# Kernel optimization log

Hardware: AMD Instinct MI355X
Metric: run time of the kernel (lower is better)

Reference implementation:

```python
import jax, jax.numpy as jnp
import numpy as np

EMB = 64  # emb_dim
T = 4     # message-passing steps


def setup_inputs() -> dict:
    key = jax.random.key(0)
    ks = jax.random.split(key, 9)
    B, N = 32, 1024
    graph = jax.random.uniform(ks[0], (B, N, N), jnp.float32)   # dense adjacency/weights
    Xv = jax.random.normal(ks[1], (B, N, 1), jnp.float32)       # per-vertex scalar feature
    s = lambda k, shp: (jax.random.normal(k, shp, jnp.float32) * 0.05)
    return {
        "graph": graph,
        "Xv": Xv,
        "W1": s(ks[2], (EMB, 1)),        # Linear(1, emb) no bias, torch layout [out, in]
        "W2": s(ks[3], (EMB, EMB)),
        "W3": s(ks[4], (EMB, EMB)),
        "W4": s(ks[5], (EMB, 1)),
        "W5": s(ks[6], (1, 2 * EMB)),
        "W6": s(ks[7], (EMB, EMB)),
        "W7": s(ks[8], (EMB, EMB)),
    }


def reference(graph, Xv, W1, W2, W3, W4, W5, W6, W7):
    B, N = Xv.shape[0], Xv.shape[1]
    # v1 = W1(Xv): [B,N,1] @ [1,EMB] -> [B,N,EMB]
    v1 = Xv @ W1.T
    # Original: v3 = W3(sum_j W4(graph[...,None])). W4 is linear (no bias), so
    # sum_j W4(g_ij) == W4(sum_j g_ij) -- exact by linearity, avoids [B,N,N,EMB] temp.
    deg = jnp.sum(graph, axis=2, keepdims=True)        # [B,N,1]
    v3 = (deg @ W4.T) @ W3.T                           # [B,N,EMB]
    base = v1 + v3                                     # loop-invariant part
    emb = jnp.zeros((B, N, EMB), dtype=Xv.dtype)
    for _ in range(T):
        neighbor_sum = jnp.einsum('bij,bjd->bid', graph, emb)  # bmm aggregation
        emb = jax.nn.relu(base + neighbor_sum @ W2.T)
    emb_sum = jnp.sum(emb, axis=1)                     # [B,EMB]
    # v6.repeat(1,N).view(B,N,EMB) == broadcast the per-graph vector to every vertex
    v6 = jnp.broadcast_to((emb_sum @ W6.T)[:, None, :], (B, N, EMB))
    v7 = emb @ W7.T
    ct = jax.nn.relu(jnp.concatenate([v6, v7], axis=2))  # [B,N,2*EMB]
    return (ct @ W5.T)[..., 0]                            # [B,N]
```

## Files before the change

kernel.cpp:

```cpp
#include <hip/hip_runtime.h>
#include <stdint.h>

#define BATCH 32
#define NV 1024
#define EMB 64

typedef __attribute__((ext_vector_type(8))) short bf16x8;
typedef __attribute__((ext_vector_type(4))) float f32x4;

__device__ __forceinline__ unsigned short f2b(float f) {
  unsigned int u = __builtin_bit_cast(unsigned int, f);
  u += 0x7fffu + ((u >> 16) & 1u);
  return (unsigned short)(u >> 16);
}
__device__ __forceinline__ float b2f(unsigned short s) {
  unsigned int u = ((unsigned int)s) << 16;
  return __builtin_bit_cast(float, u);
}

__device__ __forceinline__ void gll16(void* lds, const void* gsrc) {
  __builtin_amdgcn_global_load_lds(
      (const __attribute__((address_space(1))) unsigned int*)gsrc,
      (__attribute__((address_space(3))) unsigned int*)lds, 16, 0, 0);
}

__global__ __launch_bounds__(256) void k_prep(
    const float* __restrict__ graph, const float* __restrict__ Xv,
    const float* __restrict__ W1, const float* __restrict__ W3,
    const float* __restrict__ W4,
    unsigned short* __restrict__ G16, float* __restrict__ degp,
    float* __restrict__ w34g, unsigned short* __restrict__ embT)
{
  __shared__ float w34s[EMB];
  __shared__ __align__(16) unsigned short ebT[EMB][68];
  const int tid = threadIdx.x;
  const int b = blockIdx.x >> 4;
  const int rb = blockIdx.x & 15;
  if (tid < EMB) {
    float s = 0.f;
    const float* w3r = W3 + tid * EMB;
#pragma unroll
    for (int k = 0; k < EMB; ++k) s += w3r[k] * W4[k];
    w34s[tid] = s;
    if (blockIdx.x == 0) w34g[tid] = s;
  }
  __syncthreads();
  const int wv = tid >> 6, lane = tid & 63;
  const float w1v = W1[lane];
  const float w34v = w34s[lane];
  for (int i = 0; i < 16; ++i) {
    const int row = rb * 64 + wv * 16 + i;
    const float4* gr = (const float4*)(graph + ((size_t)b * NV + row) * NV);
    float part = 0.f;
    ushort4 outp[4];
#pragma unroll
    for (int c = 0; c < 4; ++c) {
      float4 v = gr[c * 64 + lane];
      part += (v.x + v.y) + (v.z + v.w);
      outp[c].x = f2b(v.x); outp[c].y = f2b(v.y);
      outp[c].z = f2b(v.z); outp[c].w = f2b(v.w);
    }
    ushort4* g16r = (ushort4*)(G16 + ((size_t)b * NV + row) * NV);
#pragma unroll
    for (int c = 0; c < 4; ++c) g16r[c * 64 + lane] = outp[c];
#pragma unroll
    for (int d = 1; d < 64; d <<= 1) part += __shfl_xor(part, d);
    const float deg = part;
    if (lane == 0) degp[b * NV + row] = deg;
    const float xv = Xv[b * NV + row];
    const float bs = xv * w1v + deg * w34v;
    ebT[lane][wv * 16 + i] = f2b(fmaxf(bs, 0.f));
  }
  __syncthreads();
  const int e = tid >> 2, q = tid & 3;
  ushort4* dst = (ushort4*)(embT + ((size_t)(b * EMB + e)) * NV + rb * 64 + q * 16);
  const ushort4* srcr = (const ushort4*)(&ebT[e][q * 16]);
#pragma unroll
  for (int c = 0; c < 4; ++c) dst[c] = srcr[c];
}

__global__ __launch_bounds__(256) void k_step(
    const unsigned short* __restrict__ G16,
    const unsigned short* __restrict__ embin,
    unsigned short* __restrict__ embout,
    const float* __restrict__ W2, const float* __restrict__ W1,
    const float* __restrict__ w34g, const float* __restrict__ Xv,
    const float* __restrict__ degp)
{
  __shared__ __align__(16) char lds[16384];
  char* At = lds;
  char* Bt = lds + 8192;
  const int tid = threadIdx.x;
  const int lane = tid & 63;
  const int wv = tid >> 6;
  const int wm = wv >> 1;
  const int wn = wv & 1;
  const int b = blockIdx.x >> 4;
  const int mblk = blockIdx.x & 15;
  const int l15 = lane & 15, l4 = lane >> 4;

  bf16x8 w2f[2][2];
  float w1e[2], w34e[2];
#pragma unroll
  for (int e16 = 0; e16 < 2; ++e16) {
    const int eg = wn * 32 + e16 * 16 + l15;
    w1e[e16] = W1[eg];
    w34e[e16] = w34g[eg];
#pragma unroll
    for (int kk = 0; kk < 2; ++kk) {
      const float* src = W2 + eg * 64 + kk * 32 + l4 * 8;
      bf16x8 f;
#pragma unroll
      for (int j = 0; j < 8; ++j) f[j] = (short)f2b(src[j]);
      w2f[e16][kk] = f;
    }
  }

  f32x4 acc[2][2] = {};
  const size_t gbase = ((size_t)b * NV + mblk * 64) * NV;
  const size_t ebase = (size_t)b * EMB * NV;

  for (int kt = 0; kt < 16; ++kt) {
#pragma unroll
    for (int i = 0; i < 2; ++i) {
      const int cc = i * 256 + tid;
      const int lrow = cc >> 3, lcg = cc & 7;
      const int gcg = lcg ^ (lrow & 7);
      gll16(At + (i * 256 + wv * 64) * 16,
            G16 + gbase + (size_t)lrow * NV + kt * 64 + gcg * 8);
    }
#pragma unroll
    for (int i = 0; i < 2; ++i) {
      const int cc = i * 256 + tid;
      const int er = cc >> 3, lcg = cc & 7;
      const int gcg = lcg ^ (er & 7);
      gll16(Bt + (i * 256 + wv * 64) * 16,
            embin + ebase + (size_t)er * NV + kt * 64 + gcg * 8);
    }
    __syncthreads();
#pragma unroll
    for (int kk = 0; kk < 2; ++kk) {
      bf16x8 af[2], bf[2];
      const int gq = kk * 4 + l4;
#pragma unroll
      for (int m16 = 0; m16 < 2; ++m16) {
        const int row = wm * 32 + m16 * 16 + l15;
        af[m16] = *(const bf16x8*)(At + row * 128 + ((gq ^ (row & 7)) << 4));
      }
#pragma unroll
      for (int n16 = 0; n16 < 2; ++n16) {
        const int er = wn * 32 + n16 * 16 + l15;
        bf[n16] = *(const bf16x8*)(Bt + er * 128 + ((gq ^ (er & 7)) << 4));
      }
#pragma unroll
      for (int m16 = 0; m16 < 2; ++m16)
#pragma unroll
        for (int n16 = 0; n16 < 2; ++n16)
          acc[m16][n16] = __builtin_amdgcn_mfma_f32_16x16x32_bf16(
              af[m16], bf[n16], acc[m16][n16], 0, 0, 0);
    }
    __syncthreads();
  }

#pragma unroll
  for (int m16 = 0; m16 < 2; ++m16)
#pragma unroll
    for (int n16 = 0; n16 < 2; ++n16)
#pragma unroll
      for (int r = 0; r < 4; ++r) {
        const int m = wm * 32 + m16 * 16 + l4 * 4 + r;
        const int n = wn * 32 + n16 * 16 + l15;
        const int addr = m * 128 + (((n >> 3) ^ (m & 7)) << 4) + (n & 7) * 2;
        *(unsigned short*)(At + addr) = f2b(acc[m16][n16][r]);
      }
  __syncthreads();

  f32x4 acc2[2][2] = {};
#pragma unroll
  for (int kk = 0; kk < 2; ++kk) {
    bf16x8 sa[2];
    const int gq = kk * 4 + l4;
#pragma unroll
    for (int m16 = 0; m16 < 2; ++m16) {
      const int row = wm * 32 + m16 * 16 + l15;
      sa[m16] = *(const bf16x8*)(At + row * 128 + ((gq ^ (row & 7)) << 4));
    }
#pragma unroll
    for (int m16 = 0; m16 < 2; ++m16)
#pragma unroll
      for (int e16 = 0; e16 < 2; ++e16)
        acc2[m16][e16] = __builtin_amdgcn_mfma_f32_16x16x32_bf16(
            sa[m16], w2f[e16][kk], acc2[m16][e16], 0, 0, 0);
  }

#pragma unroll
  for (int m16 = 0; m16 < 2; ++m16) {
    const int m0 = mblk * 64 + wm * 32 + m16 * 16 + l4 * 4;
    float xv[4], dg[4];
#pragma unroll
    for (int r = 0; r < 4; ++r) {
      xv[r] = Xv[b * NV + m0 + r];
      dg[r] = degp[b * NV + m0 + r];
    }
#pragma unroll
    for (int e16 = 0; e16 < 2; ++e16) {
      const int eg = wn * 32 + e16 * 16 + l15;
      ushort4 pk;
      unsigned short* pks = (unsigned short*)&pk;
#pragma unroll
      for (int r = 0; r < 4; ++r) {
        const float bs = xv[r] * w1e[e16] + dg[r] * w34e[e16];
        pks[r] = f2b(fmaxf(acc2[m16][e16][r] + bs, 0.f));
      }
      *(ushort4*)(embout + ((size_t)(b * EMB + eg)) * NV + m0) = pk;
    }
  }
}

__global__ __launch_bounds__(256) void k_red(
    const unsigned short* __restrict__ embT, const float* __restrict__ W6,
    const float* __restrict__ W5, float* __restrict__ s6)
{
  __shared__ float part[256];
  __shared__ float esum[EMB];
  const int b = blockIdx.x, tid = threadIdx.x;
  const int e = tid >> 2, q = tid & 3;
  const unsigned short* rowp = embT + ((size_t)(b * EMB + e)) * NV;
  float s = 0.f;
  for (int j = 0; j < 32; ++j) {
    const ushort4* p = (const ushort4*)(rowp + q * 8 + j * 32);
    ushort4 a = p[0], c = p[1];
    s += (b2f(a.x) + b2f(a.y)) + (b2f(a.z) + b2f(a.w)) +
         (b2f(c.x) + b2f(c.y)) + (b2f(c.z) + b2f(c.w));
  }
  part[tid] = s;
  __syncthreads();
  if (tid < EMB)
    esum[tid] = part[tid * 4] + part[tid * 4 + 1] + part[tid * 4 + 2] + part[tid * 4 + 3];
  __syncthreads();
  if (tid < EMB) {
    float v6 = 0.f;
    const float* w6r = W6 + tid * EMB;
#pragma unroll
    for (int k = 0; k < EMB; ++k) v6 += w6r[k] * esum[k];
    float contrib = W5[tid] * fmaxf(v6, 0.f);
#pragma unroll
    for (int d = 1; d < 64; d <<= 1) contrib += __shfl_xor(contrib, d);
    if (tid == 0) s6[b] = contrib;
  }
}

__global__ __launch_bounds__(256) void k_out(
    const unsigned short* __restrict__ embT, const float* __restrict__ W7,
    const float* __restrict__ W5, const float* __restrict__ s6,
    float* __restrict__ out)
{
  __shared__ __align__(16) unsigned short et[EMB][256];
  const int tid = threadIdx.x;
  const int b = blockIdx.x >> 2;
  const int n0 = (blockIdx.x & 3) * 256;
#pragma unroll
  for (int i = 0; i < 8; ++i) {
    const int c = i * 256 + tid;
    const int k = c >> 5, off = (c & 31) * 8;
    *(uint4*)&et[k][off] =
        *(const uint4*)(embT + ((size_t)(b * EMB + k)) * NV + n0 + off);
  }
  __syncthreads();
  float ev[64];
#pragma unroll
  for (int k = 0; k < 64; ++k) ev[k] = b2f(et[k][tid]);
  float s7 = 0.f;
  for (int e = 0; e < 64; ++e) {
    const float* w7r = W7 + e * 64;
    float a = 0.f;
#pragma unroll
    for (int k = 0; k < 64; ++k) a += ev[k] * w7r[k];
    s7 += W5[64 + e] * fmaxf(a, 0.f);
  }
  out[b * NV + n0 + tid] = s6[b] + s7;
}

extern "C" void kernel_launch(void* const* d_in, const int* in_sizes, int n_in,
                              void* d_out, int out_size, void* d_ws, size_t ws_size,
                              hipStream_t stream) {
  const float* graph = (const float*)d_in[0];
  const float* Xv = (const float*)d_in[1];
  const float* W1 = (const float*)d_in[2];
  const float* W2 = (const float*)d_in[3];
  const float* W3 = (const float*)d_in[4];
  const float* W4 = (const float*)d_in[5];
  const float* W5 = (const float*)d_in[6];
  const float* W6 = (const float*)d_in[7];
  const float* W7 = (const float*)d_in[8];
  float* out = (float*)d_out;
  char* ws = (char*)d_ws;

  unsigned short* G16 = (unsigned short*)ws;
  unsigned short* embA = (unsigned short*)(ws + 67108864);
  unsigned short* embB = (unsigned short*)(ws + 71303168);
  float* degp = (float*)(ws + 75497472);
  float* w34g = (float*)(ws + 75628544);
  float* s6 = (float*)(ws + 75628800);

  k_prep<<<512, 256, 0, stream>>>(graph, Xv, W1, W3, W4, G16, degp, w34g, embA);
  k_step<<<512, 256, 0, stream>>>(G16, embA, embB, W2, W1, w34g, Xv, degp);
  k_step<<<512, 256, 0, stream>>>(G16, embB, embA, W2, W1, w34g, Xv, degp);
  k_step<<<512, 256, 0, stream>>>(G16, embA, embB, W2, W1, w34g, Xv, degp);
  k_red<<<32, 256, 0, stream>>>(embB, W6, W5, s6);
  k_out<<<128, 256, 0, stream>>>(embB, W7, W5, s6, out);
}
```

Measured before the change: 309.8 us.

## Fuse all stages into one persistent kernel with grid barriers and double buffering

Replaces the six launches (prep, three steps, reduce, output) with one persistent kernel of 512 blocks that synchronises between message-passing steps using an atomic-counter grid barrier. The step GEMM's LDS staging is double-buffered so the next tile's loads overlap the current MFMA work. Degree, Xv and W3·W4 are kept in LDS, and the final step keeps its embeddings in LDS to compute the readout directly. The graph-sum reduction uses atomics into a zeroed workspace. This removes launch gaps and intermediate global traffic, but relies on all 512 blocks being co-resident (launch bounds of 2 blocks per SM) and adds a memset plus spin-wait barrier costs.

New measurement: 483.5 us. +56.1%, slower.

```diff
diff --git a/kernel.cpp b/kernel.cpp
--- a/kernel.cpp
+++ b/kernel.cpp
@@ -1,9 +1,9 @@
 #include <hip/hip_runtime.h>
 #include <stdint.h>
 
-#define BATCH 32
 #define NV 1024
 #define EMB 64
+#define NBLK 512
 
 typedef __attribute__((ext_vector_type(8))) short bf16x8;
 typedef __attribute__((ext_vector_type(4))) float f32x4;
@@ -24,80 +24,93 @@
       (__attribute__((address_space(3))) unsigned int*)lds, 16, 0, 0);
 }
 
-__global__ __launch_bounds__(256) void k_prep(
+__global__ __launch_bounds__(256, 2) void k_fused(
     const float* __restrict__ graph, const float* __restrict__ Xv,
-    const float* __restrict__ W1, const float* __restrict__ W3,
-    const float* __restrict__ W4,
-    unsigned short* __restrict__ G16, float* __restrict__ degp,
-    float* __restrict__ w34g, unsigned short* __restrict__ embT)
+    const float* __restrict__ W1, const float* __restrict__ W2,
+    const float* __restrict__ W3, const float* __restrict__ W4,
+    const float* __restrict__ W5, const float* __restrict__ W6,
+    const float* __restrict__ W7,
+    unsigned short* __restrict__ G16,
+    unsigned short* __restrict__ embA,
+    unsigned short* __restrict__ embB,
+    float* __restrict__ esum_ws, unsigned int* __restrict__ bar,
+    float* __restrict__ out)
 {
+  __shared__ __align__(16) char ldsbuf[32768];
   __shared__ float w34s[EMB];
-  __shared__ __align__(16) unsigned short ebT[EMB][68];
+  __shared__ float degs[EMB];
+  __shared__ float xvs[EMB];
+  __shared__ float esl[EMB];
+  __shared__ float redl[256];
+  __shared__ float s6l;
+
   const int tid = threadIdx.x;
+  const int lane = tid & 63;
+  const int wv = tid >> 6;
   const int b = blockIdx.x >> 4;
-  const int rb = blockIdx.x & 15;
+  const int mb = blockIdx.x & 15;
+  const int wm = wv >> 1, wn = wv & 1;
+  const int l15 = lane & 15, l4 = lane >> 4;
+
+  auto gbar = [&](unsigned int target) {
+    __syncthreads();
+    if (tid == 0) {
+      __threadfence();
+      __hip_atomic_fetch_add(bar, 1u, __ATOMIC_RELAXED, __HIP_MEMORY_SCOPE_AGENT);
+      while (__hip_atomic_load(bar, __ATOMIC_RELAXED, __HIP_MEMORY_SCOPE_AGENT) < target)
+        __builtin_amdgcn_s_sleep(2);
+      __threadfence();
+    }
+    __syncthreads();
+  };
+
   if (tid < EMB) {
     float s = 0.f;
     const float* w3r = W3 + tid * EMB;
 #pragma unroll
     for (int k = 0; k < EMB; ++k) s += w3r[k] * W4[k];
     w34s[tid] = s;
-    if (blockIdx.x == 0) w34g[tid] = s;
   }
   __syncthreads();
-  const int wv = tid >> 6, lane = tid & 63;
-  const float w1v = W1[lane];
-  const float w34v = w34s[lane];
-  for (int i = 0; i < 16; ++i) {
-    const int row = rb * 64 + wv * 16 + i;
-    const float4* gr = (const float4*)(graph + ((size_t)b * NV + row) * NV);
-    float part = 0.f;
-    ushort4 outp[4];
-#pragma unroll
-    for (int c = 0; c < 4; ++c) {
-      float4 v = gr[c * 64 + lane];
-      part += (v.x + v.y) + (v.z + v.w);
-      outp[c].x = f2b(v.x); outp[c].y = f2b(v.y);
-      outp[c].z = f2b(v.z); outp[c].w = f2b(v.w);
-    }
-    ushort4* g16r = (ushort4*)(G16 + ((size_t)b * NV + row) * NV);
-#pragma unroll
-    for (int c = 0; c < 4; ++c) g16r[c * 64 + lane] = outp[c];
-#pragma unroll
-    for (int d = 1; d < 64; d <<= 1) part += __shfl_xor(part, d);
-    const float deg = part;
-    if (lane == 0) degp[b * NV + row] = deg;
-    const float xv = Xv[b * NV + row];
-    const float bs = xv * w1v + deg * w34v;
-    ebT[lane][wv * 16 + i] = f2b(fmaxf(bs, 0.f));
-  }
-  __syncthreads();
-  const int e = tid >> 2, q = tid & 3;
-  ushort4* dst = (ushort4*)(embT + ((size_t)(b * EMB + e)) * NV + rb * 64 + q * 16);
-  const ushort4* srcr = (const ushort4*)(&ebT[e][q * 16]);
-#pragma unroll
-  for (int c = 0; c < 4; ++c) dst[c] = srcr[c];
-}
-
-__global__ __launch_bounds__(256) void k_step(
-    const unsigned short* __restrict__ G16,
-    const unsigned short* __restrict__ embin,
-    unsigned short* __restrict__ embout,
-    const float* __restrict__ W2, const float* __restrict__ W1,
-    const float* __restrict__ w34g, const float* __restrict__ Xv,
-    const float* __restrict__ degp)
-{
-  __shared__ __align__(16) char lds[16384];
-  char* At = lds;
-  char* Bt = lds + 8192;
-  const int tid = threadIdx.x;
-  const int lane = tid & 63;
-  const int wv = tid >> 6;
-  const int wm = wv >> 1;
-  const int wn = wv & 1;
-  const int b = blockIdx.x >> 4;
-  const int mblk = blockIdx.x & 15;
-  const int l15 = lane & 15, l4 = lane >> 4;
+  {
+    unsigned short* ebT = (unsigned short*)ldsbuf;
+    const float w1v = W1[lane];
+    const float w34v = w34s[lane];
+    for (int i = 0; i < 16; ++i) {
+      const int rloc = wv * 16 + i;
+      const int row = mb * 64 + rloc;
+      const float4* gr = (const float4*)(graph + ((size_t)b * NV + row) * NV);
+      float part = 0.f;
+      ushort4 outp[4];
+#pragma unroll
+      for (int c = 0; c < 4; ++c) {
+        float4 v = gr[c * 64 + lane];
+        part += (v.x + v.y) + (v.z + v.w);
+        outp[c].x = f2b(v.x); outp[c].y = f2b(v.y);
+        outp[c].z = f2b(v.z); outp[c].w = f2b(v.w);
+      }
+      ushort4* g16r = (ushort4*)(G16 + ((size_t)b * NV + row) * NV);
+#pragma unroll
+      for (int c = 0; c < 4; ++c) g16r[c * 64 + lane] = outp[c];
+#pragma unroll
+      for (int d = 1; d < 64; d <<= 1) part += __shfl_xor(part, d);
+      const float deg = part;
+      const float xv = Xv[b * NV + row];
+      if (lane == 0) { degs[rloc] = deg; xvs[rloc] = xv; }
+      const float bs = xv * w1v + deg * w34v;
+      ebT[lane * 68 + rloc] = f2b(fmaxf(bs, 0.f));
+    }
+    __syncthreads();
+    const int e = tid >> 2, q = tid & 3;
+    ushort4* dst = (ushort4*)(embA + ((size_t)(b * EMB + e)) * NV + mb * 64 + q * 16);
+    const ushort4* srcr = (const ushort4*)(ebT + e * 68 + q * 16);
+#pragma unroll
+    for (int c = 0; c < 4; ++c) dst[c] = srcr[c];
+  }
+  gbar(NBLK);
+
+  const size_t gbase = ((size_t)b * NV + mb * 64) * NV;
+  const size_t ebase = (size_t)b * EMB * NV;
 
   bf16x8 w2f[2][2];
   float w1e[2], w34e[2];
@@ -105,7 +118,7 @@
   for (int e16 = 0; e16 < 2; ++e16) {
     const int eg = wn * 32 + e16 * 16 + l15;
     w1e[e16] = W1[eg];
-    w34e[e16] = w34g[eg];
+    w34e[e16] = w34s[eg];
 #pragma unroll
     for (int kk = 0; kk < 2; ++kk) {
       const float* src = W2 + eg * 64 + kk * 32 + l4 * 8;
@@ -116,169 +129,174 @@
     }
   }
 
-  f32x4 acc[2][2] = {};
-  const size_t gbase = ((size_t)b * NV + mblk * 64) * NV;
-  const size_t ebase = (size_t)b * EMB * NV;
-
-  for (int kt = 0; kt < 16; ++kt) {
-#pragma unroll
-    for (int i = 0; i < 2; ++i) {
-      const int cc = i * 256 + tid;
-      const int lrow = cc >> 3, lcg = cc & 7;
-      const int gcg = lcg ^ (lrow & 7);
-      gll16(At + (i * 256 + wv * 64) * 16,
-            G16 + gbase + (size_t)lrow * NV + kt * 64 + gcg * 8);
-    }
-#pragma unroll
-    for (int i = 0; i < 2; ++i) {
-      const int cc = i * 256 + tid;
-      const int er = cc >> 3, lcg = cc & 7;
-      const int gcg = lcg ^ (er & 7);
-      gll16(Bt + (i * 256 + wv * 64) * 16,
-            embin + ebase + (size_t)er * NV + kt * 64 + gcg * 8);
-    }
-    __syncthreads();
+  auto do_step = [&](const unsigned short* embin, unsigned short* embout, int s) {
+    f32x4 acc[2][2] = {};
+    auto STAGE = [&](int bufi, int kt) {
+      char* Ad = ldsbuf + bufi * 16384;
+      char* Bd = Ad + 8192;
+#pragma unroll
+      for (int i = 0; i < 2; ++i) {
+        const int cc = i * 256 + tid;
+        const int lrow = cc >> 3, lcg = cc & 7;
+        const int gcg = lcg ^ (lrow & 7);
+        gll16(Ad + (i * 256 + wv * 64) * 16,
+              G16 + gbase + (size_t)lrow * NV + kt * 64 + gcg * 8);
+      }
+#pragma unroll
+      for (int i = 0; i < 2; ++i) {
+        const int cc = i * 256 + tid;
+        const int er = cc >> 3, lcg = cc & 7;
+        const int gcg = lcg ^ (er & 7);
+        gll16(Bd + (i * 256 + wv * 64) * 16,
+              embin + ebase + (size_t)er * NV + kt * 64 + gcg * 8);
+      }
+    };
+    STAGE(0, 0);
+    int cur = 0;
+    for (int kt = 0; kt < 16; ++kt) {
+      if (kt < 15) {
+        STAGE(cur ^ 1, kt + 1);
+        asm volatile("s_waitcnt vmcnt(4)" ::: "memory");
+      } else {
+        asm volatile("s_waitcnt vmcnt(0)" ::: "memory");
+      }
+      __builtin_amdgcn_s_barrier();
+      asm volatile("" ::: "memory");
+      const char* At = ldsbuf + cur * 16384;
+      const char* Bt = At + 8192;
+#pragma unroll
+      for (int kk = 0; kk < 2; ++kk) {
+        bf16x8 af[2], bf[2];
+        const int gq = kk * 4 + l4;
+#pragma unroll
+        for (int m16 = 0; m16 < 2; ++m16) {
+          const int row = wm * 32 + m16 * 16 + l15;
+          af[m16] = *(const bf16x8*)(At + row * 128 + ((gq ^ (row & 7)) << 4));
+        }
+#pragma unroll
+        for (int n16 = 0; n16 < 2; ++n16) {
+          const int er = wn * 32 + n16 * 16 + l15;
+          bf[n16] = *(const bf16x8*)(Bt + er * 128 + ((gq ^ (er & 7)) << 4));
+        }
+#pragma unroll
+        for (int m16 = 0; m16 < 2; ++m16)
+#pragma unroll
+          for (int n16 = 0; n16 < 2; ++n16)
+            acc[m16][n16] = __builtin_amdgcn_mfma_f32_16x16x32_bf16(
+                af[m16], bf[n16], acc[m16][n16], 0, 0, 0);
+      }
+      asm volatile("" ::: "memory");
+      __builtin_amdgcn_s_barrier();
+      cur ^= 1;
+    }
+
+    char* St = ldsbuf;
+    if (s == 3 && tid < 64) esl[tid] = 0.f;
+#pragma unroll
+    for (int m16 = 0; m16 < 2; ++m16)
+#pragma unroll
+      for (int n16 = 0; n16 < 2; ++n16)
+#pragma unroll
+        for (int r = 0; r < 4; ++r) {
+          const int m = wm * 32 + m16 * 16 + l4 * 4 + r;
+          const int n = wn * 32 + n16 * 16 + l15;
+          const int addr = m * 128 + (((n >> 3) ^ (m & 7)) << 4) + (n & 7) * 2;
+          *(unsigned short*)(St + addr) = f2b(acc[m16][n16][r]);
+        }
+    __syncthreads();
+
+    f32x4 acc2[2][2] = {};
 #pragma unroll
     for (int kk = 0; kk < 2; ++kk) {
-      bf16x8 af[2], bf[2];
+      bf16x8 sa[2];
       const int gq = kk * 4 + l4;
 #pragma unroll
       for (int m16 = 0; m16 < 2; ++m16) {
         const int row = wm * 32 + m16 * 16 + l15;
-        af[m16] = *(const bf16x8*)(At + row * 128 + ((gq ^ (row & 7)) << 4));
-      }
-#pragma unroll
-      for (int n16 = 0; n16 < 2; ++n16) {
-        const int er = wn * 32 + n16 * 16 + l15;
-        bf[n16] = *(const bf16x8*)(Bt + er * 128 + ((gq ^ (er & 7)) << 4));
+        sa[m16] = *(const bf16x8*)(St + row * 128 + ((gq ^ (row & 7)) << 4));
       }
 #pragma unroll
       for (int m16 = 0; m16 < 2; ++m16)
 #pragma unroll
-        for (int n16 = 0; n16 < 2; ++n16)
-          acc[m16][n16] = __builtin_amdgcn_mfma_f32_16x16x32_bf16(
-              af[m16], bf[n16], acc[m16][n16], 0, 0, 0);
-    }
-    __syncthreads();
-  }
-
-#pragma unroll
-  for (int m16 = 0; m16 < 2; ++m16)
-#pragma unroll
-    for (int n16 = 0; n16 < 2; ++n16)
-#pragma unroll
-      for (int r = 0; r < 4; ++r) {
-        const int m = wm * 32 + m16 * 16 + l4 * 4 + r;
-        const int n = wn * 32 + n16 * 16 + l15;
-        const int addr = m * 128 + (((n >> 3) ^ (m & 7)) << 4) + (n & 7) * 2;
-        *(unsigned short*)(At + addr) = f2b(acc[m16][n16][r]);
-      }
-  __syncthreads();
-
-  f32x4 acc2[2][2] = {};
-#pragma unroll
-  for (int kk = 0; kk < 2; ++kk) {
-    bf16x8 sa[2];
-    const int gq = kk * 4 + l4;
+        for (int e16 = 0; e16 < 2; ++e16)
+          acc2[m16][e16] = __builtin_amdgcn_mfma_f32_16x16x32_bf16(
+              sa[m16], w2f[e16][kk], acc2[m16][e16], 0, 0, 0);
+    }
+
+    float* et = (float*)(ldsbuf + 8192);
 #pragma unroll
     for (int m16 = 0; m16 < 2; ++m16) {
-      const int row = wm * 32 + m16 * 16 + l15;
-      sa[m16] = *(const bf16x8*)(At + row * 128 + ((gq ^ (row & 7)) << 4));
-    }
-#pragma unroll
-    for (int m16 = 0; m16 < 2; ++m16)
-#pragma unroll
-      for (int e16 = 0; e16 < 2; ++e16)
-        acc2[m16][e16] = __builtin_amdgcn_mfma_f32_16x16x32_bf16(
-            sa[m16], w2f[e16][kk], acc2[m16][e16], 0, 0, 0);
-  }
-
-#pragma unroll
-  for (int m16 = 0; m16 < 2; ++m16) {
-    const int m0 = mblk * 64 + wm * 32 + m16 * 16 + l4 * 4;
-    float xv[4], dg[4];
-#pragma unroll
-    for (int r = 0; r < 4; ++r) {
-      xv[r] = Xv[b * NV + m0 + r];
-      dg[r] = degp[b * NV + m0 + r];
-    }
-#pragma unroll
-    for (int e16 = 0; e16 < 2; ++e16) {
-      const int eg = wn * 32 + e16 * 16 + l15;
-      ushort4 pk;
-      unsigned short* pks = (unsigned short*)&pk;
-#pragma unroll
-      for (int r = 0; r < 4; ++r) {
-        const float bs = xv[r] * w1e[e16] + dg[r] * w34e[e16];
-        pks[r] = f2b(fmaxf(acc2[m16][e16][r] + bs, 0.f));
-      }
-      *(ushort4*)(embout + ((size_t)(b * EMB + eg)) * NV + m0) = pk;
-    }
-  }
-}
-
-__global__ __launch_bounds__(256) void k_red(
-    const unsigned short* __restrict__ embT, const float* __restrict__ W6,
-    const float* __restrict__ W5, float* __restrict__ s6)
-{
-  __shared__ float part[256];
-  __shared__ float esum[EMB];
-  const int b = blockIdx.x, tid = threadIdx.x;
-  const int e = tid >> 2, q = tid & 3;
-  const unsigned short* rowp = embT + ((size_t)(b * EMB + e)) * NV;
-  float s = 0.f;
-  for (int j = 0; j < 32; ++j) {
-    const ushort4* p = (const ushort4*)(rowp + q * 8 + j * 32);
-    ushort4 a = p[0], c = p[1];
-    s += (b2f(a.x) + b2f(a.y)) + (b2f(a.z) + b2f(a.w)) +
-         (b2f(c.x) + b2f(c.y)) + (b2f(c.z) + b2f(c.w));
-  }
-  part[tid] = s;
-  __syncthreads();
-  if (tid < EMB)
-    esum[tid] = part[tid * 4] + part[tid * 4 + 1] + part[tid * 4 + 2] + part[tid * 4 + 3];
-  __syncthreads();
-  if (tid < EMB) {
+      const int ml0 = wm * 32 + m16 * 16 + l4 * 4;
+      float xv4[4], dg4[4];
+#pragma unroll
+      for (int r = 0; r < 4; ++r) { xv4[r] = xvs[ml0 + r]; dg4[r] = degs[ml0 + r]; }
+#pragma unroll
+      for (int e16 = 0; e16 < 2; ++e16) {
+        const int eg = wn * 32 + e16 * 16 + l15;
+        if (s < 3) {
+          ushort4 pk;
+          unsigned short* pks = (unsigned short*)&pk;
+#pragma unroll
+          for (int r = 0; r < 4; ++r) {
+            const float bs = xv4[r] * w1e[e16] + dg4[r] * w34e[e16];
+            pks[r] = f2b(fmaxf(acc2[m16][e16][r] + bs, 0.f));
+          }
+          *(ushort4*)(embout + ((size_t)(b * EMB + eg)) * NV + mb * 64 + ml0) = pk;
+        } else {
+          float evs = 0.f;
+#pragma unroll
+          for (int r = 0; r < 4; ++r) {
+            const float bs = xv4[r] * w1e[e16] + dg4[r] * w34e[e16];
+            const float val = fmaxf(acc2[m16][e16][r] + bs, 0.f);
+            et[(ml0 + r) * 65 + eg] = val;
+            evs += val;
+          }
+          atomicAdd(&esl[eg], evs);
+        }
+      }
+    }
+    if (s == 3) {
+      __syncthreads();
+      if (tid < 64) atomicAdd(&esum_ws[b * EMB + tid], esl[tid]);
+    }
+  };
+
+  do_step(embA, embB, 1);  gbar(2 * NBLK);
+  do_step(embB, embA, 2);  gbar(3 * NBLK);
+  do_step(embA, embB, 3);  gbar(4 * NBLK);
+
+  if (tid < 64) {
+    const float* es = esum_ws + b * EMB;
     float v6 = 0.f;
     const float* w6r = W6 + tid * EMB;
 #pragma unroll
-    for (int k = 0; k < EMB; ++k) v6 += w6r[k] * esum[k];
-    float contrib = W5[tid] * fmaxf(v6, 0.f);
-#pragma unroll
-    for (int d = 1; d < 64; d <<= 1) contrib += __shfl_xor(contrib, d);
-    if (tid == 0) s6[b] = contrib;
-  }
-}
-
-__global__ __launch_bounds__(256) void k_out(
-    const unsigned short* __restrict__ embT, const float* __restrict__ W7,
-    const float* __restrict__ W5, const float* __restrict__ s6,
-    float* __restrict__ out)
-{
-  __shared__ __align__(16) unsigned short et[EMB][256];
-  const int tid = threadIdx.x;
-  const int b = blockIdx.x >> 2;
-  const int n0 = (blockIdx.x & 3) * 256;
-#pragma unroll
-  for (int i = 0; i < 8; ++i) {
-    const int c = i * 256 + tid;
-    const int k = c >> 5, off = (c & 31) * 8;
-    *(uint4*)&et[k][off] =
-        *(const uint4*)(embT + ((size_t)(b * EMB + k)) * NV + n0 + off);
+    for (int k = 0; k < EMB; ++k) v6 += w6r[k] * es[k];
+    float c = W5[tid] * fmaxf(v6, 0.f);
+#pragma unroll
+    for (int d = 1; d < 64; d <<= 1) c += __shfl_xor(c, d);
+    if (tid == 0) s6l = c;
   }
   __syncthreads();
-  float ev[64];
-#pragma unroll
-  for (int k = 0; k < 64; ++k) ev[k] = b2f(et[k][tid]);
-  float s7 = 0.f;
-  for (int e = 0; e < 64; ++e) {
-    const float* w7r = W7 + e * 64;
-    float a = 0.f;
-#pragma unroll
-    for (int k = 0; k < 64; ++k) a += ev[k] * w7r[k];
-    s7 += W5[64 + e] * fmaxf(a, 0.f);
-  }
-  out[b * NV + n0 + tid] = s6[b] + s7;
+  {
+    const float* et = (const float*)(ldsbuf + 8192);
+    const int v = tid & 63, eq = tid >> 6;
+    float ev[64];
+#pragma unroll
+    for (int k = 0; k < EMB; ++k) ev[k] = et[v * 65 + k];
+    float sp = 0.f;
+    for (int e = eq * 16; e < eq * 16 + 16; ++e) {
+      const float* w7r = W7 + e * 64;
+      float a = 0.f;
+#pragma unroll
+      for (int k = 0; k < 64; ++k) a += ev[k] * w7r[k];
+      sp += W5[64 + e] * fmaxf(a, 0.f);
+    }
+    redl[tid] = sp;
+    __syncthreads();
+    if (tid < 64)
+      out[b * NV + mb * 64 + tid] =
+          s6l + redl[tid] + redl[tid + 64] + redl[tid + 128] + redl[tid + 192];
+  }
 }
 
 extern "C" void kernel_launch(void* const* d_in, const int* in_sizes, int n_in,
@@ -297,16 +315,13 @@
   char* ws = (char*)d_ws;
 
   unsigned short* G16 = (unsigned short*)ws;
-  unsigned short* embA = (unsigned short*)(ws + 67108864);
-  unsigned short* embB = (unsigned short*)(ws + 71303168);
-  float* degp = (float*)(ws + 75497472);
-  float* w34g = (float*)(ws + 75628544);
-  float* s6 = (float*)(ws + 75628800);
-
-  k_prep<<<512, 256, 0, stream>>>(graph, Xv, W1, W3, W4, G16, degp, w34g, embA);
-  k_step<<<512, 256, 0, stream>>>(G16, embA, embB, W2, W1, w34g, Xv, degp);
-  k_step<<<512, 256, 0, stream>>>(G16, embB, embA, W2, W1, w34g, Xv, degp);
-  k_step<<<512, 256, 0, stream>>>(G16, embA, embB, W2, W1, w34g, Xv, degp);
-  k_red<<<32, 256, 0, stream>>>(embB, W6, W5, s6);
-  k_out<<<128, 256, 0, stream>>>(embB, W7, W5, s6, out);
-}
+  unsigned short* embA = (unsigned short*)(ws + (64u << 20));
+  unsigned short* embB = (unsigned short*)(ws + (68u << 20));
+  char* ctrl = ws + (72u << 20);
+  unsigned int* bar = (unsigned int*)ctrl;
+  float* esum_ws = (float*)(ctrl + 64);
+
+  hipMemsetAsync(ctrl, 0, 64 + 32 * 64 * 4, stream);
+  k_fused<<<NBLK, 256, 0, stream>>>(graph, Xv, W1, W2, W3, W4, W5, W6, W7,
+                                    G16, embA, embB, esum_ws, bar, out);
+}
```

## Triple-buffer step kernel loads, swizzle blocks across XCDs, fuse reduction into last step

Applied to the files above, without the earlier changes.

The step kernel now prefetches the graph and embedding tiles into a three-deep LDS ring using explicit vmcnt waits and raw barriers, so global loads overlap the MFMA work. Blocks are remapped so consecutive IDs land on different XCDs while sharing the same batch per XCD, which is meant to improve L2 locality for the shared embedding tile. The separate reduction kernel is removed: the last step accumulates per-graph embedding sums through LDS and global atomics, and the output kernel computes the v6 term itself. The cost is more LDS per block, atomic contention, a memset launch, and summation order that varies from run to run.

Result: faster. 296.8 us (-4.2%).

```diff
diff --git a/kernel.cpp b/kernel.cpp
--- a/kernel.cpp
+++ b/kernel.cpp
@@ -1,7 +1,6 @@
 #include <hip/hip_runtime.h>
 #include <stdint.h>
 
-#define BATCH 32
 #define NV 1024
 #define EMB 64
 
@@ -22,6 +21,12 @@
   __builtin_amdgcn_global_load_lds(
       (const __attribute__((address_space(1))) unsigned int*)gsrc,
       (__attribute__((address_space(3))) unsigned int*)lds, 16, 0, 0);
+}
+
+__device__ __forceinline__ void swz(int j, int& b, int& mb) {
+  const int xcd = j & 7, s = j >> 3;
+  b = xcd + 8 * (s >> 4);
+  mb = s & 15;
 }
 
 __global__ __launch_bounds__(256) void k_prep(
@@ -34,8 +39,7 @@
   __shared__ float w34s[EMB];
   __shared__ __align__(16) unsigned short ebT[EMB][68];
   const int tid = threadIdx.x;
-  const int b = blockIdx.x >> 4;
-  const int rb = blockIdx.x & 15;
+  int b, mb; swz(blockIdx.x, b, mb);
   if (tid < EMB) {
     float s = 0.f;
     const float* w3r = W3 + tid * EMB;
@@ -49,7 +53,8 @@
   const float w1v = W1[lane];
   const float w34v = w34s[lane];
   for (int i = 0; i < 16; ++i) {
-    const int row = rb * 64 + wv * 16 + i;
+    const int rloc = wv * 16 + i;
+    const int row = mb * 64 + rloc;
     const float4* gr = (const float4*)(graph + ((size_t)b * NV + row) * NV);
     float part = 0.f;
     ushort4 outp[4];
@@ -69,34 +74,32 @@
     if (lane == 0) degp[b * NV + row] = deg;
     const float xv = Xv[b * NV + row];
     const float bs = xv * w1v + deg * w34v;
-    ebT[lane][wv * 16 + i] = f2b(fmaxf(bs, 0.f));
+    ebT[lane][rloc] = f2b(fmaxf(bs, 0.f));
   }
   __syncthreads();
   const int e = tid >> 2, q = tid & 3;
-  ushort4* dst = (ushort4*)(embT + ((size_t)(b * EMB + e)) * NV + rb * 64 + q * 16);
+  ushort4* dst = (ushort4*)(embT + ((size_t)(b * EMB + e)) * NV + mb * 64 + q * 16);
   const ushort4* srcr = (const ushort4*)(&ebT[e][q * 16]);
 #pragma unroll
   for (int c = 0; c < 4; ++c) dst[c] = srcr[c];
 }
 
-__global__ __launch_bounds__(256) void k_step(
+template <int LAST>
+__global__ __launch_bounds__(256, 4) void k_step(
     const unsigned short* __restrict__ G16,
     const unsigned short* __restrict__ embin,
     unsigned short* __restrict__ embout,
     const float* __restrict__ W2, const float* __restrict__ W1,
     const float* __restrict__ w34g, const float* __restrict__ Xv,
-    const float* __restrict__ degp)
+    const float* __restrict__ degp, float* __restrict__ esum_ws)
 {
-  __shared__ __align__(16) char lds[16384];
-  char* At = lds;
-  char* Bt = lds + 8192;
+  __shared__ __align__(16) char ldsbuf[49152];
+  __shared__ float esl[EMB];
   const int tid = threadIdx.x;
   const int lane = tid & 63;
   const int wv = tid >> 6;
-  const int wm = wv >> 1;
-  const int wn = wv & 1;
-  const int b = blockIdx.x >> 4;
-  const int mblk = blockIdx.x & 15;
+  int b, mb; swz(blockIdx.x, b, mb);
+  const int wm = wv >> 1, wn = wv & 1;
   const int l15 = lane & 15, l4 = lane >> 4;
 
   bf16x8 w2f[2][2];
@@ -115,18 +118,21 @@
       w2f[e16][kk] = f;
     }
   }
+  if (LAST && tid < EMB) esl[tid] = 0.f;
 
   f32x4 acc[2][2] = {};
-  const size_t gbase = ((size_t)b * NV + mblk * 64) * NV;
+  const size_t gbase = ((size_t)b * NV + mb * 64) * NV;
   const size_t ebase = (size_t)b * EMB * NV;
 
-  for (int kt = 0; kt < 16; ++kt) {
+  auto STAGE = [&](int bufi, int kt) {
+    char* Ad = ldsbuf + bufi * 16384;
+    char* Bd = Ad + 8192;
 #pragma unroll
     for (int i = 0; i < 2; ++i) {
       const int cc = i * 256 + tid;
       const int lrow = cc >> 3, lcg = cc & 7;
       const int gcg = lcg ^ (lrow & 7);
-      gll16(At + (i * 256 + wv * 64) * 16,
+      gll16(Ad + (i * 256 + wv * 64) * 16,
             G16 + gbase + (size_t)lrow * NV + kt * 64 + gcg * 8);
     }
 #pragma unroll
@@ -134,13 +140,29 @@
       const int cc = i * 256 + tid;
       const int er = cc >> 3, lcg = cc & 7;
       const int gcg = lcg ^ (er & 7);
-      gll16(Bt + (i * 256 + wv * 64) * 16,
+      gll16(Bd + (i * 256 + wv * 64) * 16,
             embin + ebase + (size_t)er * NV + kt * 64 + gcg * 8);
     }
-    __syncthreads();
+  };
+
+  STAGE(0, 0);
+  STAGE(1, 1);
+  for (int kt = 0; kt < 16; ++kt) {
+    if (kt < 14) {
+      STAGE((kt + 2) % 3, kt + 2);
+      asm volatile("s_waitcnt vmcnt(8)" ::: "memory");
+    } else if (kt == 14) {
+      asm volatile("s_waitcnt vmcnt(4)" ::: "memory");
+    } else {
+      asm volatile("s_waitcnt vmcnt(0)" ::: "memory");
+    }
+    __builtin_amdgcn_s_barrier();
+    asm volatile("" ::: "memory");
+    const char* At = ldsbuf + (kt % 3) * 16384;
+    const char* Bt = At + 8192;
 #pragma unroll
     for (int kk = 0; kk < 2; ++kk) {
-      bf16x8 af[2], bf[2];
+      bf16x8 af[2], bfr[2];
       const int gq = kk * 4 + l4;
 #pragma unroll
       for (int m16 = 0; m16 < 2; ++m16) {
@@ -150,18 +172,20 @@
 #pragma unroll
       for (int n16 = 0; n16 < 2; ++n16) {
         const int er = wn * 32 + n16 * 16 + l15;
-        bf[n16] = *(const bf16x8*)(Bt + er * 128 + ((gq ^ (er & 7)) << 4));
+        bfr[n16] = *(const bf16x8*)(Bt + er * 128 + ((gq ^ (er & 7)) << 4));
       }
 #pragma unroll
       for (int m16 = 0; m16 < 2; ++m16)
 #pragma unroll
         for (int n16 = 0; n16 < 2; ++n16)
           acc[m16][n16] = __builtin_amdgcn_mfma_f32_16x16x32_bf16(
-              af[m16], bf[n16], acc[m16][n16], 0, 0, 0);
-    }
-    __syncthreads();
-  }
-
+              af[m16], bfr[n16], acc[m16][n16], 0, 0, 0);
+    }
+    asm volatile("" ::: "memory");
+    __builtin_amdgcn_s_barrier();
+  }
+
+  char* St = ldsbuf;
 #pragma unroll
   for (int m16 = 0; m16 < 2; ++m16)
 #pragma unroll
@@ -171,7 +195,7 @@
         const int m = wm * 32 + m16 * 16 + l4 * 4 + r;
         const int n = wn * 32 + n16 * 16 + l15;
         const int addr = m * 128 + (((n >> 3) ^ (m & 7)) << 4) + (n & 7) * 2;
-        *(unsigned short*)(At + addr) = f2b(acc[m16][n16][r]);
+        *(unsigned short*)(St + addr) = f2b(acc[m16][n16][r]);
       }
   __syncthreads();
 
@@ -183,7 +207,7 @@
 #pragma unroll
     for (int m16 = 0; m16 < 2; ++m16) {
       const int row = wm * 32 + m16 * 16 + l15;
-      sa[m16] = *(const bf16x8*)(At + row * 128 + ((gq ^ (row & 7)) << 4));
+      sa[m16] = *(const bf16x8*)(St + row * 128 + ((gq ^ (row & 7)) << 4));
     }
 #pragma unroll
     for (int m16 = 0; m16 < 2; ++m16)
@@ -195,67 +219,44 @@
 
 #pragma unroll
   for (int m16 = 0; m16 < 2; ++m16) {
-    const int m0 = mblk * 64 + wm * 32 + m16 * 16 + l4 * 4;
-    float xv[4], dg[4];
+    const int ml0 = wm * 32 + m16 * 16 + l4 * 4;
+    const int m0 = mb * 64 + ml0;
+    float xv4[4], dg4[4];
 #pragma unroll
     for (int r = 0; r < 4; ++r) {
-      xv[r] = Xv[b * NV + m0 + r];
-      dg[r] = degp[b * NV + m0 + r];
+      xv4[r] = Xv[b * NV + m0 + r];
+      dg4[r] = degp[b * NV + m0 + r];
     }
 #pragma unroll
     for (int e16 = 0; e16 < 2; ++e16) {
       const int eg = wn * 32 + e16 * 16 + l15;
       ushort4 pk;
       unsigned short* pks = (unsigned short*)&pk;
+      float evs = 0.f;
 #pragma unroll
       for (int r = 0; r < 4; ++r) {
-        const float bs = xv[r] * w1e[e16] + dg[r] * w34e[e16];
-        pks[r] = f2b(fmaxf(acc2[m16][e16][r] + bs, 0.f));
+        const float bs = xv4[r] * w1e[e16] + dg4[r] * w34e[e16];
+        const float val = fmaxf(acc2[m16][e16][r] + bs, 0.f);
+        pks[r] = f2b(val);
+        evs += val;
       }
       *(ushort4*)(embout + ((size_t)(b * EMB + eg)) * NV + m0) = pk;
-    }
-  }
-}
-
-__global__ __launch_bounds__(256) void k_red(
-    const unsigned short* __restrict__ embT, const float* __restrict__ W6,
-    const float* __restrict__ W5, float* __restrict__ s6)
-{
-  __shared__ float part[256];
-  __shared__ float esum[EMB];
-  const int b = blockIdx.x, tid = threadIdx.x;
-  const int e = tid >> 2, q = tid & 3;
-  const unsigned short* rowp = embT + ((size_t)(b * EMB + e)) * NV;
-  float s = 0.f;
-  for (int j = 0; j < 32; ++j) {
-    const ushort4* p = (const ushort4*)(rowp + q * 8 + j * 32);
-    ushort4 a = p[0], c = p[1];
-    s += (b2f(a.x) + b2f(a.y)) + (b2f(a.z) + b2f(a.w)) +
-         (b2f(c.x) + b2f(c.y)) + (b2f(c.z) + b2f(c.w));
-  }
-  part[tid] = s;
-  __syncthreads();
-  if (tid < EMB)
-    esum[tid] = part[tid * 4] + part[tid * 4 + 1] + part[tid * 4 + 2] + part[tid * 4 + 3];
-  __syncthreads();
-  if (tid < EMB) {
-    float v6 = 0.f;
-    const float* w6r = W6 + tid * EMB;
-#pragma unroll
-    for (int k = 0; k < EMB; ++k) v6 += w6r[k] * esum[k];
-    float contrib = W5[tid] * fmaxf(v6, 0.f);
-#pragma unroll
-    for (int d = 1; d < 64; d <<= 1) contrib += __shfl_xor(contrib, d);
-    if (tid == 0) s6[b] = contrib;
+      if (LAST) atomicAdd(&esl[eg], evs);
+    }
+  }
+  if (LAST) {
+    __syncthreads();
+    if (tid < EMB) atomicAdd(&esum_ws[b * EMB + tid], esl[tid]);
   }
 }
 
 __global__ __launch_bounds__(256) void k_out(
     const unsigned short* __restrict__ embT, const float* __restrict__ W7,
-    const float* __restrict__ W5, const float* __restrict__ s6,
-    float* __restrict__ out)
+    const float* __restrict__ W5, const float* __restrict__ W6,
+    const float* __restrict__ esum_ws, float* __restrict__ out)
 {
   __shared__ __align__(16) unsigned short et[EMB][256];
+  __shared__ float s6l;
   const int tid = threadIdx.x;
   const int b = blockIdx.x >> 2;
   const int n0 = (blockIdx.x & 3) * 256;
@@ -266,6 +267,17 @@
     *(uint4*)&et[k][off] =
         *(const uint4*)(embT + ((size_t)(b * EMB + k)) * NV + n0 + off);
   }
+  if (tid < EMB) {
+    const float* es = esum_ws + b * EMB;
+    float v6 = 0.f;
+    const float* w6r = W6 + tid * EMB;
+#pragma unroll
+    for (int k = 0; k < EMB; ++k) v6 += w6r[k] * es[k];
+    float c = W5[tid] * fmaxf(v6, 0.f);
+#pragma unroll
+    for (int d = 1; d < 64; d <<= 1) c += __shfl_xor(c, d);
+    if (tid == 0) s6l = c;
+  }
   __syncthreads();
   float ev[64];
 #pragma unroll
@@ -278,7 +290,7 @@
     for (int k = 0; k < 64; ++k) a += ev[k] * w7r[k];
     s7 += W5[64 + e] * fmaxf(a, 0.f);
   }
-  out[b * NV + n0 + tid] = s6[b] + s7;
+  out[b * NV + n0 + tid] = s6l + s7;
 }
 
 extern "C" void kernel_launch(void* const* d_in, const int* in_sizes, int n_in,
@@ -297,16 +309,16 @@
   char* ws = (char*)d_ws;
 
   unsigned short* G16 = (unsigned short*)ws;
-  unsigned short* embA = (unsigned short*)(ws + 67108864);
-  unsigned short* embB = (unsigned short*)(ws + 71303168);
-  float* degp = (float*)(ws + 75497472);
-  float* w34g = (float*)(ws + 75628544);
-  float* s6 = (float*)(ws + 75628800);
-
+  unsigned short* embA = (unsigned short*)(ws + (64u << 20));
+  unsigned short* embB = (unsigned short*)(ws + (68u << 20));
+  float* degp = (float*)(ws + (72u << 20));
+  float* w34g = (float*)(ws + (72u << 20) + (128u << 10));
+  float* esum_ws = (float*)(ws + (72u << 20) + (130u << 10));
+
+  hipMemsetAsync(esum_ws, 0, 32 * EMB * sizeof(float), stream);
   k_prep<<<512, 256, 0, stream>>>(graph, Xv, W1, W3, W4, G16, degp, w34g, embA);
-  k_step<<<512, 256, 0, stream>>>(G16, embA, embB, W2, W1, w34g, Xv, degp);
-  k_step<<<512, 256, 0, stream>>>(G16, embB, embA, W2, W1, w34g, Xv, degp);
-  k_step<<<512, 256, 0, stream>>>(G16, embA, embB, W2, W1, w34g, Xv, degp);
-  k_red<<<32, 256, 0, stream>>>(embB, W6, W5, s6);
-  k_out<<<128, 256, 0, stream>>>(embB, W7, W5, s6, out);
-}
+  k_step<0><<<512, 256, 0, stream>>>(G16, embA, embB, W2, W1, w34g, Xv, degp, esum_ws);
+  k_step<0><<<512, 256, 0, stream>>>(G16, embB, embA, W2, W1, w34g, Xv, degp, esum_ws);
+  k_step<1><<<512, 256, 0, stream>>>(G16, embA, embB, W2, W1, w34g, Xv, degp, esum_ws);
+  k_out<<<128, 256, 0, stream>>>(embB, W7, W5, W6, esum_ws, out);
+}
```
